# Kernel optimization log

Hardware: AMD Instinct MI355X
Metric: run time of the kernel (lower is better)

## Reference

```python
import jax, jax.numpy as jnp
import numpy as np
from jax import lax

H = 256          # hidden_size
VOCAB = 30000
N_OPS = 9
N_COLS = 16
T = 4            # num_time_steps
Q = 64           # question length
N_NUM = 8        # numbers appearing in the question
ROWS = 1_000_000

# operation indices (Neural Programmer, ICLR 2016 op set)
OP_SUM, OP_COUNT, OP_DIFF, OP_GREATER, OP_LESSER, OP_AND, OP_OR, OP_ASSIGN, OP_RESET = range(N_OPS)


def setup_inputs() -> dict:
    key = jax.random.key(0)
    ks = jax.random.split(key, 13)
    s = 0.05
    f32 = jnp.float32
    return {
        "input_question": jax.random.randint(ks[0], (Q,), 0, VOCAB),
        "input_question_numbers": jax.random.randint(ks[1], (N_NUM,), 0, 100),
        "left_word_indices": jax.random.randint(ks[2], (N_NUM,), 0, Q),
        "table": jax.random.normal(ks[3], (ROWS, N_COLS), f32),
        # learned parameters
        "emb": jax.random.normal(ks[4], (VOCAB, H), f32) * s,      # question word embeddings
        "Wx": jax.random.normal(ks[5], (H, H), f32) * s,           # question RNN input weight
        "Wh": jax.random.normal(ks[6], (H, H), f32) * s,           # question RNN recurrent weight
        "W_op": jax.random.normal(ks[7], (H, 2 * H), f32) * s,     # selector (op branch)
        "op_emb": jax.random.normal(ks[8], (N_OPS, H), f32) * s,   # operation embeddings
        "W_col": jax.random.normal(ks[9], (H, 2 * H), f32) * s,    # selector (column branch)
        "col_emb": jax.random.normal(ks[10], (N_COLS, H), f32) * s,# column embeddings
        "W_hist": jax.random.normal(ks[11], (H, 3 * H), f32) * s,  # history RNN
        "U": jax.random.normal(ks[12], (2, H), f32) * s,           # lesser/greater pivot vectors
    }


def reference(input_question, input_question_numbers, left_word_indices, table,
              emb, Wx, Wh, W_op, op_emb, W_col, col_emb, W_hist, U):
    dt = table.dtype
    hid = Wx.shape[0]

    # ---- question RNN (simple tanh RNN) ----
    xs = emb[input_question]                               # [Q, H]
    def step(h, x):
        h2 = jnp.tanh(x @ Wx.T + h @ Wh.T)
        return h2, h2
    q, hs = lax.scan(step, jnp.zeros((hid,), dt), xs)      # q=[H], hs=[Q,H]

    # ---- pivot computation (z_matrix = hidden states left of each number) ----
    z = hs[left_word_indices]                              # [N_NUM, H]
    nums = input_question_numbers.astype(dt)               # [N_NUM]
    l_pivot = jax.nn.softmax(z @ U[0]) @ nums              # scalar
    g_pivot = jax.nn.softmax(z @ U[1]) @ nums              # scalar

    # soft comparison maps (pivots are timestep-independent; compute once)
    sel_l = jax.nn.sigmoid(l_pivot - table)                # [R, C] ~ [table < l_pivot]
    sel_g = jax.nn.sigmoid(table - g_pivot)                # [R, C] ~ [table > g_pivot]

    h_hist = jnp.zeros((hid,), dt)
    scalars = [jnp.zeros((), dt)]
    rs_list = [jnp.ones((table.shape[0],), dt)]
    lookup = jnp.zeros(table.shape, dt)

    for _ in range(T):
        rs1 = rs_list[-1]
        rs2 = rs_list[max(0, len(rs_list) - 2)]
        s1 = scalars[-1]
        s3 = scalars[max(0, len(scalars) - 3)]

        # selector: soft op / column distributions from [question; history]
        qh = jnp.concatenate([q, h_hist])                  # [2H]
        a_op = jax.nn.softmax(op_emb @ jnp.tanh(W_op @ qh))    # [N_OPS]
        a_col = jax.nn.softmax(col_emb @ jnp.tanh(W_col @ qh)) # [N_COLS]

        # row select (soft mixture over ops)
        rs = (a_op[OP_GREATER] * (sel_g @ a_col)
              + a_op[OP_LESSER] * (sel_l @ a_col)
              + a_op[OP_AND] * jnp.minimum(rs1, rs2)
              + a_op[OP_OR] * jnp.maximum(rs1, rs2)
              + a_op[OP_RESET] * jnp.ones_like(rs1)
              + (a_op[OP_SUM] + a_op[OP_COUNT] + a_op[OP_DIFF] + a_op[OP_ASSIGN]) * rs1)

        # scalar answer
        scalar = (a_op[OP_SUM] * jnp.sum(rs1 @ table)
                  + a_op[OP_COUNT] * jnp.sum(rs1)
                  + a_op[OP_DIFF] * (s3 - s1))

        # lookup answer: assign op prints selected rows/columns
        lookup = a_op[OP_ASSIGN] * rs[:, None] * a_col[None, :]

        # history RNN
        c = jnp.concatenate([a_op @ op_emb, a_col @ col_emb, h_hist])  # [3H]
        h_hist = jnp.tanh(W_hist @ c)

        rs_list.append(rs)
        scalars.append(scalar)

    return scalars[-1], lookup
```

## Files before the change

### kernel.cpp

```cpp
#include <hip/hip_runtime.h>
#include <hip/hip_fp16.h>
#include <math.h>

#define HDIM   256
#define QLEN   64
#define NNUM   8
#define NOPS   9
#define NCOLS  16
#define TSTEPS 4


#define WS_LPIV 0
#define WS_GPIV 1
#define WS_ACOL 2
#define WS_AOP  66
#define WS_Q    112
#define WS_PQO  368
#define WS_PQC  624
#define WS_HS   880
#define WS_XP   2928
#define WS_AH   19312
#define WS_BH   21616
#define WS_WH16 25712
#define WS_M16  58480
#define WS_PART 156784
#define NBLK_C  2048

typedef _Float16 f16x8 __attribute__((ext_vector_type(8)));
typedef _Float16 f16x4 __attribute__((ext_vector_type(4)));
typedef float    f32x4 __attribute__((ext_vector_type(4)));

__device__ __forceinline__ float fast_tanh(float x) {
    return 1.0f - 2.0f / (__expf(2.0f * x) + 1.0f);
}

__global__ void precompute_kernel(const int* __restrict__ q,
                                  const float* __restrict__ emb,
                                  const float* __restrict__ Wx,
                                  const float* __restrict__ Wh,
                                  float* __restrict__ ws) {
    int gid = blockIdx.x * 256 + threadIdx.x;
    if (gid < QLEN * HDIM) {
        int t = gid >> 8, j = gid & 255;
        const float4* x4 = (const float4*)(emb + (size_t)q[t] * HDIM);
        const float4* w4 = (const float4*)(Wx + (size_t)j * HDIM);
        float s = 0.f;
        for (int k = 0; k < HDIM / 4; k++) {
            float4 a = x4[k], b = w4[k];
            s += a.x * b.x + a.y * b.y + a.z * b.z + a.w * b.w;
        }
        ws[WS_XP + t * HDIM + j] = s;
    } else {
        int did = gid - QLEN * HDIM;
        int hidx = did * 2;
        int e = hidx & 7, qr = (hidx >> 3) & 15, quad = (hidx >> 7) & 3;
        int kk = (hidx >> 9) & 7, t = hidx >> 12;
        const float* src = Wh + (size_t)(16 * t + qr) * HDIM + kk * 32 + quad * 8 + e;
        float2 v = *(const float2*)src;
        ((__half2*)(ws + WS_WH16))[did] = __floats2half2_rn(v.x, v.y);
    }
}

__global__ __launch_bounds__(256, 1) void rnn_kernel(
        float* __restrict__ ws,
        const int* __restrict__ lwi,
        const float* __restrict__ W_op,
        const float* __restrict__ W_col,
        const float* __restrict__ W_hist,
        const float* __restrict__ op_emb,
        const float* __restrict__ col_emb) {
    if (blockIdx.x != 0) {
        int gid = (blockIdx.x - 1) * 256 + threadIdx.x;
        if (gid < HDIM * NOPS) {
            int j = gid / NOPS, o = gid % NOPS;
            const float4* w4 = (const float4*)(W_hist + (size_t)j * (3 * HDIM));
            const float4* e4 = (const float4*)(op_emb + (size_t)o * HDIM);
            float s = 0.f;
            for (int k = 0; k < HDIM / 4; k++) {
                float4 a = w4[k], b = e4[k];
                s += a.x * b.x + a.y * b.y + a.z * b.z + a.w * b.w;
            }
            ws[WS_AH + gid] = s;
        } else if (gid < HDIM * NOPS + HDIM * NCOLS) {
            int idx = gid - HDIM * NOPS;
            int j = idx / NCOLS, c = idx % NCOLS;
            const float4* w4 = (const float4*)(W_hist + (size_t)j * (3 * HDIM) + HDIM);
            const float4* e4 = (const float4*)(col_emb + (size_t)c * HDIM);
            float s = 0.f;
            for (int k = 0; k < HDIM / 4; k++) {
                float4 a = w4[k], b = e4[k];
                s += a.x * b.x + a.y * b.y + a.z * b.z + a.w * b.w;
            }
            ws[WS_BH + idx] = s;
        } else if (gid < HDIM * NOPS + HDIM * NCOLS + 98304) {
            int did = gid - (HDIM * NOPS + HDIM * NCOLS);
            int mat = did >> 15;
            int hidx = (did & 32767) * 2;
            int e = hidx & 7, j = (hidx >> 3) & 255, i = hidx >> 11;
            const float* src;
            if (mat == 0)      src = W_op   + (size_t)j * (2 * HDIM) + HDIM     + i * 8 + e;
            else if (mat == 1) src = W_col  + (size_t)j * (2 * HDIM) + HDIM     + i * 8 + e;
            else               src = W_hist + (size_t)j * (3 * HDIM) + 2 * HDIM + i * 8 + e;
            float2 v = *(const float2*)src;
            ((__half2*)(ws + WS_M16))[did] = __floats2half2_rn(v.x, v.y);
        }
        return;
    }

    __shared__ float xpL[QLEN * HDIM];
    __shared__ _Float16 hF[2][HDIM];
    __shared__ unsigned stepmask[QLEN];

    const int tid = threadIdx.x;
    const int wave = tid >> 6, lane = tid & 63;
    const int quad = lane >> 4, qr = lane & 15;
    const int myrow = 64 * wave + 16 * (qr >> 2) + quad * 4 + (qr & 3);

    #pragma unroll
    for (int i = 0; i < 16; i++) {
        int idx = (i * 256 + tid) * 4;
        *(float4*)(xpL + idx) = *(const float4*)(ws + WS_XP + idx);
    }
    if (tid < QLEN) {
        unsigned m = 0;
        #pragma unroll
        for (int i = 0; i < NNUM; i++) m |= (lwi[i] == tid) ? (1u << i) : 0u;
        stepmask[tid] = m;
    }
    const _Float16* wsh = (const _Float16*)(ws + WS_WH16);
    f16x8 aW[4][8];
    #pragma unroll
    for (int r = 0; r < 4; r++)
        #pragma unroll
        for (int kk = 0; kk < 8; kk++)
            aW[r][kk] = *(const f16x8*)(wsh + ((size_t)(((4 * wave + r) * 8 + kk) * 64 + lane)) * 8);
    #pragma unroll
    for (int r = 0; r < 4; r++)
        #pragma unroll
        for (int kk = 0; kk < 8; kk++) {
            f32x4 t = __builtin_bit_cast(f32x4, aW[r][kk]);
            asm volatile("" : "+v"(t));
            aW[r][kk] = __builtin_bit_cast(f16x8, t);
        }
    hF[0][tid] = (_Float16)0.f;
    __syncthreads();

    for (int s = 0; s < QLEN; s++) {
        const _Float16* hb = hF[s & 1];
        f16x8 bfrag[8];
        #pragma unroll
        for (int kk = 0; kk < 8; kk++)
            bfrag[kk] = *(const f16x8*)(hb + kk * 32 + quad * 8);
        f32x4 acc[4];
        #pragma unroll
        for (int r = 0; r < 4; r++) acc[r] = (f32x4){0.f, 0.f, 0.f, 0.f};
        #pragma unroll
        for (int kk = 0; kk < 8; kk++)
            #pragma unroll
            for (int r = 0; r < 4; r++)
                acc[r] = __builtin_amdgcn_mfma_f32_16x16x32_f16(aW[r][kk], bfrag[kk], acc[r], 0, 0, 0);

        f32x4 t01 = (qr & 4) ? acc[1] : acc[0];
        f32x4 t23 = (qr & 4) ? acc[3] : acc[2];
        f32x4 tt  = (qr & 8) ? t23 : t01;
        float e01 = (qr & 1) ? tt.y : tt.x;
        float e23 = (qr & 1) ? tt.w : tt.z;
        float v   = (qr & 2) ? e23 : e01;

        float h = fast_tanh(v + xpL[s * HDIM + myrow]);
        hF[(s + 1) & 1][myrow] = (_Float16)h;
        unsigned m = stepmask[s];
        while (m) {
            int i = __builtin_ctz(m);
            ws[WS_HS + i * HDIM + myrow] = h;
            m &= m - 1;
        }
        if (s == QLEN - 1) ws[WS_Q + myrow] = h;
        __syncthreads();
    }
}

__global__ void qproj_kernel(const float* __restrict__ W_op,
                             const float* __restrict__ W_col,
                             float* __restrict__ ws) {
    int gid = blockIdx.x * 256 + threadIdx.x;
    int dot = gid >> 5, l = gid & 31;
    int mat = dot >> 8, j = dot & 255;
    const float* w = (mat ? W_col : W_op) + (size_t)j * (2 * HDIM) + l * 8;
    const float* qv = ws + WS_Q + l * 8;
    float4 a0 = *(const float4*)w,        a1 = *(const float4*)(w + 4);
    float4 b0 = *(const float4*)qv,       b1 = *(const float4*)(qv + 4);
    float s = a0.x * b0.x + a0.y * b0.y + a0.z * b0.z + a0.w * b0.w
            + a1.x * b1.x + a1.y * b1.y + a1.z * b1.z + a1.w * b1.w;
    s += __shfl_xor(s, 1); s += __shfl_xor(s, 2); s += __shfl_xor(s, 4);
    s += __shfl_xor(s, 8); s += __shfl_xor(s, 16);
    if (l == 0) ws[(mat ? WS_PQC : WS_PQO) + j] = s;
}

__global__ __launch_bounds__(256) void select_kernel(
        float* __restrict__ ws,
        const float* __restrict__ U,
        const int* __restrict__ nums,
        const float* __restrict__ op_emb,
        const float* __restrict__ col_emb) {
    __shared__ float zu[16];
    __shared__ float hH[HDIM];
    __shared__ float top_op[HDIM], top_col[HDIM], mh[HDIM];
    __shared__ float logits[32];
    __shared__ float aop_s[NOPS], acol_s[NCOLS];

    const int tid = threadIdx.x;

    {
        int g = tid >> 4, l = tid & 15;
        int i = g >> 1, u = g & 1;
        const float* z = ws + WS_HS + i * HDIM + l * 16;
        const float* uu = U + u * HDIM + l * 16;
        float s = 0.f;
        #pragma unroll
        for (int k = 0; k < 4; k++) {
            float4 a = *(const float4*)(z + k * 4), b = *(const float4*)(uu + k * 4);
            s += a.x * b.x + a.y * b.y + a.z * b.z + a.w * b.w;
        }
        s += __shfl_xor(s, 1); s += __shfl_xor(s, 2);
        s += __shfl_xor(s, 4); s += __shfl_xor(s, 8);
        if (l == 0) zu[g] = s;
    }
    if (tid < HDIM) hH[tid] = 0.f;
    __syncthreads();
    if (tid == 0) {
        #pragma unroll
        for (int u = 0; u < 2; u++) {
            float mx = -1e30f;
            for (int i = 0; i < NNUM; i++) mx = fmaxf(mx, zu[i * 2 + u]);
            float se = 0.f, pv = 0.f;
            for (int i = 0; i < NNUM; i++) {
                float e = __expf(zu[i * 2 + u] - mx);
                se += e;
                pv += e * (float)nums[i];
            }
            ws[u] = pv / se;
        }
    }
    __syncthreads();

    const _Float16* wsm = (const _Float16*)(ws + WS_M16);
    const float pqo = ws[WS_PQO + tid];
    const float pqc = ws[WS_PQC + tid];

    for (int t = 0; t < TSTEPS; t++) {
        float so = 0.f, sc = 0.f, sh = 0.f;
        #pragma unroll
        for (int i = 0; i < 32; i++) {
            float4 h0 = *(const float4*)(hH + i * 8);
            float4 h1 = *(const float4*)(hH + i * 8 + 4);
            f16x8 a = *(const f16x8*)(wsm + ((size_t)(0 * 32 + i) * 256 + tid) * 8);
            f16x8 b = *(const f16x8*)(wsm + ((size_t)(1 * 32 + i) * 256 + tid) * 8);
            f16x8 c = *(const f16x8*)(wsm + ((size_t)(2 * 32 + i) * 256 + tid) * 8);
            so += (float)a[0]*h0.x + (float)a[1]*h0.y + (float)a[2]*h0.z + (float)a[3]*h0.w
                + (float)a[4]*h1.x + (float)a[5]*h1.y + (float)a[6]*h1.z + (float)a[7]*h1.w;
            sc += (float)b[0]*h0.x + (float)b[1]*h0.y + (float)b[2]*h0.z + (float)b[3]*h0.w
                + (float)b[4]*h1.x + (float)b[5]*h1.y + (float)b[6]*h1.z + (float)b[7]*h1.w;
            sh += (float)c[0]*h0.x + (float)c[1]*h0.y + (float)c[2]*h0.z + (float)c[3]*h0.w
                + (float)c[4]*h1.x + (float)c[5]*h1.y + (float)c[6]*h1.z + (float)c[7]*h1.w;
        }
        top_op[tid]  = fast_tanh(pqo + so);
        top_col[tid] = fast_tanh(pqc + sc);
        mh[tid] = sh;
        __syncthreads();

        #pragma unroll
        for (int d0 = 0; d0 < 32; d0 += 8) {
            int d = d0 + (tid >> 5), l = tid & 31;
            if (d < 25) {
                float s = 0.f;
                if (d < NOPS) {
                    const float* e = op_emb + (size_t)d * HDIM;
                    #pragma unroll
                    for (int m = 0; m < 8; m++) s += e[l * 8 + m] * top_op[l * 8 + m];
                } else {
                    const float* e = col_emb + (size_t)(d - NOPS) * HDIM;
                    #pragma unroll
                    for (int m = 0; m < 8; m++) s += e[l * 8 + m] * top_col[l * 8 + m];
                }
                s += __shfl_xor(s, 1); s += __shfl_xor(s, 2); s += __shfl_xor(s, 4);
                s += __shfl_xor(s, 8); s += __shfl_xor(s, 16);
                if (l == 0) logits[d] = s;
            }
        }
        __syncthreads();
        if (tid == 0) {
            float mx = -1e30f;
            for (int o = 0; o < NOPS; o++) mx = fmaxf(mx, logits[o]);
            float se = 0.f, e[NOPS];
            for (int o = 0; o < NOPS; o++) { e[o] = __expf(logits[o] - mx); se += e[o]; }
            for (int o = 0; o < NOPS; o++) {
                float a = e[o] / se;
                aop_s[o] = a;
                ws[WS_AOP + t * NOPS + o] = a;
            }
        } else if (tid == 32) {
            float mx = -1e30f;
            for (int c = 0; c < NCOLS; c++) mx = fmaxf(mx, logits[NOPS + c]);
            float se = 0.f, e[NCOLS];
            for (int c = 0; c < NCOLS; c++) { e[c] = __expf(logits[NOPS + c] - mx); se += e[c]; }
            for (int c = 0; c < NCOLS; c++) {
                float a = e[c] / se;
                acol_s[c] = a;
                ws[WS_ACOL + t * NCOLS + c] = a;
            }
        }
        __syncthreads();
        {
            float s = mh[tid];
            const float* ah = ws + WS_AH + tid * NOPS;
            #pragma unroll
            for (int o = 0; o < NOPS; o++) s += ah[o] * aop_s[o];
            const float* bh = ws + WS_BH + tid * NCOLS;
            #pragma unroll
            for (int c = 0; c < NCOLS; c++) s += bh[c] * acol_s[c];
            float hv = fast_tanh(s);
            __syncthreads();
            hH[tid] = hv;
        }
        __syncthreads();
    }
}

__global__ __launch_bounds__(256) void table_kernel(
        const float* __restrict__ table,
        const float* __restrict__ wsc,
        float* __restrict__ wspart,
        float* __restrict__ out,
        int rows) {
    const int tid = threadIdx.x;
    const int cq = tid & 3;
    const float lpiv = wsc[WS_LPIV];
    const float gpiv = wsc[WS_GPIV];
    float4 acol4[TSTEPS];
    float wg[TSTEPS], wl[TSTEPS], wand[TSTEPS], wor[TSTEPS], wrst[TSTEPS], wpass[TSTEPS];
    #pragma unroll
    for (int t = 0; t < TSTEPS; t++) {
        acol4[t] = make_float4(wsc[WS_ACOL + t * NCOLS + cq * 4 + 0],
                               wsc[WS_ACOL + t * NCOLS + cq * 4 + 1],
                               wsc[WS_ACOL + t * NCOLS + cq * 4 + 2],
                               wsc[WS_ACOL + t * NCOLS + cq * 4 + 3]);
        wg[t]   = wsc[WS_AOP + t * NOPS + 3];
        wl[t]   = wsc[WS_AOP + t * NOPS + 4];
        wand[t] = wsc[WS_AOP + t * NOPS + 5];
        wor[t]  = wsc[WS_AOP + t * NOPS + 6];
        wrst[t] = wsc[WS_AOP + t * NOPS + 8];
        wpass[t] = wsc[WS_AOP + t * NOPS + 0] + wsc[WS_AOP + t * NOPS + 1]
                 + wsc[WS_AOP + t * NOPS + 2] + wsc[WS_AOP + t * NOPS + 7];
    }
    const float wassign = wsc[WS_AOP + 3 * NOPS + 7];

    float dAcc[TSTEPS] = {0.f, 0.f, 0.f, 0.f};
    float nAcc[TSTEPS] = {0.f, 0.f, 0.f, 0.f};
    const long rowsL = rows;

    for (long r0 = (long)blockIdx.x * 64; r0 < rowsL; r0 += (long)NBLK_C * 64) {
        long row = r0 + (tid >> 2);
        bool valid = row < rowsL;
        f32x4 tv = {0.f, 0.f, 0.f, 0.f};
        if (valid)
            tv = __builtin_nontemporal_load((const f32x4*)(table + row * NCOLS + cq * 4));
        float prs = tv.x + tv.y + tv.z + tv.w;
        float pg[4], pl[4];
        {
            float c0 = tv.x, c1 = tv.y, c2 = tv.z, c3 = tv.w;
            float sg0 = __builtin_amdgcn_rcpf(1.f + __expf(gpiv - c0));
            float sg1 = __builtin_amdgcn_rcpf(1.f + __expf(gpiv - c1));
            float sg2 = __builtin_amdgcn_rcpf(1.f + __expf(gpiv - c2));
            float sg3 = __builtin_amdgcn_rcpf(1.f + __expf(gpiv - c3));
            float sl0 = __builtin_amdgcn_rcpf(1.f + __expf(c0 - lpiv));
            float sl1 = __builtin_amdgcn_rcpf(1.f + __expf(c1 - lpiv));
            float sl2 = __builtin_amdgcn_rcpf(1.f + __expf(c2 - lpiv));
            float sl3 = __builtin_amdgcn_rcpf(1.f + __expf(c3 - lpiv));
            #pragma unroll
            for (int t = 0; t < TSTEPS; t++) {
                pg[t] = sg0 * acol4[t].x + sg1 * acol4[t].y + sg2 * acol4[t].z + sg3 * acol4[t].w;
                pl[t] = sl0 * acol4[t].x + sl1 * acol4[t].y + sl2 * acol4[t].z + sl3 * acol4[t].w;
            }
        }
        prs += __shfl_xor(prs, 1); prs += __shfl_xor(prs, 2);
        #pragma unroll
        for (int t = 0; t < TSTEPS; t++) {
            pg[t] += __shfl_xor(pg[t], 1); pg[t] += __shfl_xor(pg[t], 2);
            pl[t] += __shfl_xor(pl[t], 1); pl[t] += __shfl_xor(pl[t], 2);
        }
        float rs1 = 1.f, rs2 = 1.f;
        float vf = valid ? 1.f : 0.f;
        #pragma unroll
        for (int i = 0; i < TSTEPS; i++) {
            dAcc[i] += vf * rs1 * prs;
            nAcc[i] += vf * rs1;
            float nrs = wg[i] * pg[i] + wl[i] * pl[i]
                      + wand[i] * fminf(rs1, rs2) + wor[i] * fmaxf(rs1, rs2)
                      + wrst[i] + wpass[i] * rs1;
            rs2 = rs1;
            rs1 = nrs;
        }
        if (valid) {
            float wa = wassign * rs1;
            float* ob = out + 1 + row * NCOLS + cq * 4;
            __builtin_nontemporal_store(wa * acol4[3].x, ob + 0);
            __builtin_nontemporal_store(wa * acol4[3].y, ob + 1);
            __builtin_nontemporal_store(wa * acol4[3].z, ob + 2);
            __builtin_nontemporal_store(wa * acol4[3].w, ob + 3);
        }
    }

    #pragma unroll
    for (int i = 0; i < TSTEPS; i++) {
        #pragma unroll
        for (int off = 32; off >= 1; off >>= 1) {
            dAcc[i] += __shfl_xor(dAcc[i], off);
            nAcc[i] += __shfl_xor(nAcc[i], off);
        }
    }
    __shared__ float redl[4][8];
    int wv = tid >> 6, ln = tid & 63;
    if (ln == 0) {
        #pragma unroll
        for (int i = 0; i < TSTEPS; i++) {
            redl[wv][i] = dAcc[i];
            redl[wv][4 + i] = nAcc[i];
        }
    }
    __syncthreads();
    if (tid < 8) {
        float s = redl[0][tid] + redl[1][tid] + redl[2][tid] + redl[3][tid];
        wspart[blockIdx.x * 8 + tid] = 0.25f * s;
    }
}

__global__ void finalize_kernel(const float* __restrict__ ws, float* __restrict__ out) {
    __shared__ float red[8];
    int a = threadIdx.x >> 5, l = threadIdx.x & 31;
    float s = 0.f;
    for (int b = l; b < NBLK_C; b += 32) s += ws[WS_PART + b * 8 + a];
    s += __shfl_xor(s, 1, 32); s += __shfl_xor(s, 2, 32); s += __shfl_xor(s, 4, 32);
    s += __shfl_xor(s, 8, 32); s += __shfl_xor(s, 16, 32);
    if (l == 0) red[a] = s;
    __syncthreads();
    if (threadIdx.x == 0) {
        float Dv[4] = {red[0], red[1], red[2], red[3]};
        float Nv[4] = {red[4], red[5], red[6], red[7]};
        const float* aop = ws + WS_AOP;
        float sc[5];
        sc[0] = 0.f;
        #pragma unroll
        for (int i = 0; i < 4; i++) {
            float s1 = sc[i];
            float s3 = sc[(i >= 2) ? (i - 2) : 0];
            sc[i + 1] = aop[i * NOPS + 0] * Dv[i] + aop[i * NOPS + 1] * Nv[i]
                      + aop[i * NOPS + 2] * (s3 - s1);
        }
        out[0] = sc[4];
    }
}

extern "C" void kernel_launch(void* const* d_in, const int* in_sizes, int n_in,
                              void* d_out, int out_size, void* d_ws, size_t ws_size,
                              hipStream_t stream) {
    const int*   q       = (const int*)d_in[0];
    const int*   nums    = (const int*)d_in[1];
    const int*   lwi     = (const int*)d_in[2];
    const float* table   = (const float*)d_in[3];
    const float* emb     = (const float*)d_in[4];
    const float* Wx      = (const float*)d_in[5];
    const float* Wh      = (const float*)d_in[6];
    const float* W_op    = (const float*)d_in[7];
    const float* op_emb  = (const float*)d_in[8];
    const float* W_col   = (const float*)d_in[9];
    const float* col_emb = (const float*)d_in[10];
    const float* W_hist  = (const float*)d_in[11];
    const float* U       = (const float*)d_in[12];
    float* out = (float*)d_out;
    float* ws  = (float*)d_ws;
    int rows = in_sizes[3] / NCOLS;

    precompute_kernel<<<192, 256, 0, stream>>>(q, emb, Wx, Wh, ws);
    const int pre2_threads = HDIM * NOPS + HDIM * NCOLS + 98304;
    rnn_kernel<<<1 + (pre2_threads + 255) / 256, 256, 0, stream>>>(
        ws, lwi, W_op, W_col, W_hist, op_emb, col_emb);
    qproj_kernel<<<64, 256, 0, stream>>>(W_op, W_col, ws);
    select_kernel<<<1, 256, 0, stream>>>(ws, U, nums, op_emb, col_emb);
    table_kernel<<<NBLK_C, 256, 0, stream>>>(
        table, ws, ws + WS_PART, out, rows);
    finalize_kernel<<<1, 256, 0, stream>>>(ws, out);
}
```

Before: 264.9 us.

## Prefetch table into cache during RNN kernel and process one row per thread

Adds 2048 extra blocks to the serial RNN kernel that stream the whole table and discard the sum. The goal is to pull the 64 MB table into the MI355X's large last-level cache while the single-block RNN runs, so the later table pass reads from cache. The table kernel now gives each thread one full row, which removes the cross-lane shuffle reductions. Output stores are staged through shared memory to keep writes coalesced, at the cost of two barriers per iteration. The prefetch blocks compete with the RNN block for bandwidth, and the benefit depends on the table staying resident in cache.

```diff
diff --git a/kernel.cpp b/kernel.cpp
--- a/kernel.cpp
+++ b/kernel.cpp
@@ -25,6 +25,7 @@
 #define WS_M16  58480
 #define WS_PART 156784
 #define NBLK_C  2048
+#define PRE2_BLOCKS 409
 
 typedef _Float16 f16x8 __attribute__((ext_vector_type(8)));
 typedef _Float16 f16x4 __attribute__((ext_vector_type(4)));
@@ -68,7 +69,19 @@
         const float* __restrict__ W_col,
         const float* __restrict__ W_hist,
         const float* __restrict__ op_emb,
-        const float* __restrict__ col_emb) {
+        const float* __restrict__ col_emb,
+        const float* __restrict__ table,
+        int rows) {
+    if (blockIdx.x >= 1 + PRE2_BLOCKS) {
+        int wid = blockIdx.x - 1 - PRE2_BLOCKS;
+        const f32x4* t4 = (const f32x4*)table;
+        long n4 = (long)rows * (NCOLS / 4);
+        f32x4 acc = {0.f, 0.f, 0.f, 0.f};
+        for (long i = (long)wid * 256 + threadIdx.x; i < n4; i += (long)2048 * 256)
+            acc += t4[i];
+        asm volatile("" :: "v"(acc));
+        return;
+    }
     if (blockIdx.x != 0) {
         int gid = (blockIdx.x - 1) * 256 + threadIdx.x;
         if (gid < HDIM * NOPS) {
@@ -334,17 +347,18 @@
         float* __restrict__ out,
         int rows) {
     const int tid = threadIdx.x;
-    const int cq = tid & 3;
     const float lpiv = wsc[WS_LPIV];
     const float gpiv = wsc[WS_GPIV];
-    float4 acol4[TSTEPS];
+    float4 ac[TSTEPS][4];
     float wg[TSTEPS], wl[TSTEPS], wand[TSTEPS], wor[TSTEPS], wrst[TSTEPS], wpass[TSTEPS];
     #pragma unroll
     for (int t = 0; t < TSTEPS; t++) {
-        acol4[t] = make_float4(wsc[WS_ACOL + t * NCOLS + cq * 4 + 0],
-                               wsc[WS_ACOL + t * NCOLS + cq * 4 + 1],
-                               wsc[WS_ACOL + t * NCOLS + cq * 4 + 2],
-                               wsc[WS_ACOL + t * NCOLS + cq * 4 + 3]);
+        #pragma unroll
+        for (int g = 0; g < 4; g++)
+            ac[t][g] = make_float4(wsc[WS_ACOL + t * NCOLS + g * 4 + 0],
+                                   wsc[WS_ACOL + t * NCOLS + g * 4 + 1],
+                                   wsc[WS_ACOL + t * NCOLS + g * 4 + 2],
+                                   wsc[WS_ACOL + t * NCOLS + g * 4 + 3]);
         wg[t]   = wsc[WS_AOP + t * NOPS + 3];
         wl[t]   = wsc[WS_AOP + t * NOPS + 4];
         wand[t] = wsc[WS_AOP + t * NOPS + 5];
@@ -354,20 +368,30 @@
                  + wsc[WS_AOP + t * NOPS + 2] + wsc[WS_AOP + t * NOPS + 7];
     }
     const float wassign = wsc[WS_AOP + 3 * NOPS + 7];
-
+    const int cq = tid & 3;
+    float4 a3s = (cq & 2) ? ((cq & 1) ? ac[3][3] : ac[3][2])
+                          : ((cq & 1) ? ac[3][1] : ac[3][0]);
+
+    __shared__ float waL[256];
     float dAcc[TSTEPS] = {0.f, 0.f, 0.f, 0.f};
     float nAcc[TSTEPS] = {0.f, 0.f, 0.f, 0.f};
     const long rowsL = rows;
 
-    for (long r0 = (long)blockIdx.x * 64; r0 < rowsL; r0 += (long)NBLK_C * 64) {
-        long row = r0 + (tid >> 2);
+    for (long r0 = (long)blockIdx.x * 256; r0 < rowsL; r0 += (long)NBLK_C * 256) {
+        long row = r0 + tid;
         bool valid = row < rowsL;
-        f32x4 tv = {0.f, 0.f, 0.f, 0.f};
-        if (valid)
-            tv = __builtin_nontemporal_load((const f32x4*)(table + row * NCOLS + cq * 4));
-        float prs = tv.x + tv.y + tv.z + tv.w;
-        float pg[4], pl[4];
-        {
+        f32x4 tv0 = {0.f,0.f,0.f,0.f}, tv1 = tv0, tv2 = tv0, tv3 = tv0;
+        if (valid) {
+            const f32x4* tp = (const f32x4*)(table + row * NCOLS);
+            tv0 = tp[0]; tv1 = tp[1]; tv2 = tp[2]; tv3 = tp[3];
+        }
+        float prs = tv0.x+tv0.y+tv0.z+tv0.w + tv1.x+tv1.y+tv1.z+tv1.w
+                  + tv2.x+tv2.y+tv2.z+tv2.w + tv3.x+tv3.y+tv3.z+tv3.w;
+        float pg[TSTEPS] = {0.f,0.f,0.f,0.f};
+        float pl[TSTEPS] = {0.f,0.f,0.f,0.f};
+        #pragma unroll
+        for (int g = 0; g < 4; g++) {
+            f32x4 tv = (g == 0) ? tv0 : (g == 1) ? tv1 : (g == 2) ? tv2 : tv3;
             float c0 = tv.x, c1 = tv.y, c2 = tv.z, c3 = tv.w;
             float sg0 = __builtin_amdgcn_rcpf(1.f + __expf(gpiv - c0));
             float sg1 = __builtin_amdgcn_rcpf(1.f + __expf(gpiv - c1));
@@ -379,15 +403,9 @@
             float sl3 = __builtin_amdgcn_rcpf(1.f + __expf(c3 - lpiv));
             #pragma unroll
             for (int t = 0; t < TSTEPS; t++) {
-                pg[t] = sg0 * acol4[t].x + sg1 * acol4[t].y + sg2 * acol4[t].z + sg3 * acol4[t].w;
-                pl[t] = sl0 * acol4[t].x + sl1 * acol4[t].y + sl2 * acol4[t].z + sl3 * acol4[t].w;
-            }
-        }
-        prs += __shfl_xor(prs, 1); prs += __shfl_xor(prs, 2);
-        #pragma unroll
-        for (int t = 0; t < TSTEPS; t++) {
-            pg[t] += __shfl_xor(pg[t], 1); pg[t] += __shfl_xor(pg[t], 2);
-            pl[t] += __shfl_xor(pl[t], 1); pl[t] += __shfl_xor(pl[t], 2);
+                pg[t] += sg0*ac[t][g].x + sg1*ac[t][g].y + sg2*ac[t][g].z + sg3*ac[t][g].w;
+                pl[t] += sl0*ac[t][g].x + sl1*ac[t][g].y + sl2*ac[t][g].z + sl3*ac[t][g].w;
+            }
         }
         float rs1 = 1.f, rs2 = 1.f;
         float vf = valid ? 1.f : 0.f;
@@ -401,14 +419,25 @@
             rs2 = rs1;
             rs1 = nrs;
         }
-        if (valid) {
-            float wa = wassign * rs1;
-            float* ob = out + 1 + row * NCOLS + cq * 4;
-            __builtin_nontemporal_store(wa * acol4[3].x, ob + 0);
-            __builtin_nontemporal_store(wa * acol4[3].y, ob + 1);
-            __builtin_nontemporal_store(wa * acol4[3].z, ob + 2);
-            __builtin_nontemporal_store(wa * acol4[3].w, ob + 3);
-        }
+        waL[tid] = vf * (wassign * rs1);
+        __syncthreads();
+        {
+            int rq = tid >> 2;
+            #pragma unroll
+            for (int g = 0; g < 4; g++) {
+                int lrow = g * 64 + rq;
+                long row2 = r0 + lrow;
+                if (row2 < rowsL) {
+                    float wa2 = waL[lrow];
+                    float* ob = out + 1 + row2 * NCOLS + cq * 4;
+                    __builtin_nontemporal_store(wa2 * a3s.x, ob + 0);
+                    __builtin_nontemporal_store(wa2 * a3s.y, ob + 1);
+                    __builtin_nontemporal_store(wa2 * a3s.z, ob + 2);
+                    __builtin_nontemporal_store(wa2 * a3s.w, ob + 3);
+                }
+            }
+        }
+        __syncthreads();
     }
 
     #pragma unroll
@@ -431,7 +460,7 @@
     __syncthreads();
     if (tid < 8) {
         float s = redl[0][tid] + redl[1][tid] + redl[2][tid] + redl[3][tid];
-        wspart[blockIdx.x * 8 + tid] = 0.25f * s;
+        wspart[blockIdx.x * 8 + tid] = s;
     }
 }
 
@@ -482,9 +511,8 @@
     int rows = in_sizes[3] / NCOLS;
 
     precompute_kernel<<<192, 256, 0, stream>>>(q, emb, Wx, Wh, ws);
-    const int pre2_threads = HDIM * NOPS + HDIM * NCOLS + 98304;
-    rnn_kernel<<<1 + (pre2_threads + 255) / 256, 256, 0, stream>>>(
-        ws, lwi, W_op, W_col, W_hist, op_emb, col_emb);
+    rnn_kernel<<<1 + PRE2_BLOCKS + 2048, 256, 0, stream>>>(
+        ws, lwi, W_op, W_col, W_hist, op_emb, col_emb, table, rows);
     qproj_kernel<<<64, 256, 0, stream>>>(W_op, W_col, ws);
     select_kernel<<<1, 256, 0, stream>>>(ws, U, nums, op_emb, col_emb);
     table_kernel<<<NBLK_C, 256, 0, stream>>>(
```

Result: slower. 281.3 us (+6.2%).
